# Performance work log

Hardware: AMD Instinct MI355X
Metric: run time of the kernel (lower is better)

The kernel has to match this reference:

```python
import jax, jax.numpy as jnp
import numpy as np

B, C, H, W = 8, 512, 96, 96
C8 = C // 8


def conv1x1(x, w, b):
    # x: (B,Cin,H,W), w: (Cout,Cin), b: (Cout,)
    return jnp.einsum('bchw,oc->bohw', x, w) + b[None, :, None, None]


def setup_inputs() -> dict:
    key = jax.random.key(0)
    ks = jax.random.split(key, 12)
    s = 0.05
    return {
        'x_exmplar': jax.random.normal(ks[0], (B, C, H, W), jnp.float32),
        'x_query': jax.random.normal(ks[1], (B, C, H, W), jnp.float32),
        'Wq': jax.random.normal(ks[2], (C8, C), jnp.float32) * s,
        'bq': jax.random.normal(ks[3], (C8,), jnp.float32) * s,
        'Wk': jax.random.normal(ks[4], (C8, C), jnp.float32) * s,
        'bk': jax.random.normal(ks[5], (C8,), jnp.float32) * s,
        'Wv': jax.random.normal(ks[6], (C, C), jnp.float32) * s,
        'bv': jax.random.normal(ks[7], (C,), jnp.float32) * s,
        'Wqv': jax.random.normal(ks[8], (C, C), jnp.float32) * s,
        'bqv': jax.random.normal(ks[9], (C,), jnp.float32) * s,
        'gamma1': jax.random.normal(ks[10], (1,), jnp.float32) * 0.5,
        'gamma2': jax.random.normal(ks[11], (1,), jnp.float32) * 0.5,
    }


def reference(x_exmplar, x_query, Wq, bq, Wk, bk, Wv, bv, Wqv, bqv, gamma1, gamma2):
    Bq, Cq, Hh, Ww = x_query.shape
    q = conv1x1(x_query, Wq, bq)        # (B,C8,H,W)
    k = conv1x1(x_exmplar, Wk, bk)      # (B,C8,H,W)
    v = conv1x1(x_exmplar, Wv, bv)      # (B,C,H,W)
    qv = conv1x1(x_query, Wqv, bqv)     # (B,C,H,W)

    # Criss-cross energies. energy_H masks the self position (INF diag).
    eH = jnp.einsum('bchw,bcjw->bhwj', q, k)            # (B,H,W,H)
    eye = jnp.eye(Hh, dtype=bool)                        # (H,H)
    eH = jnp.where(eye[:, None, :], -jnp.inf, eH)        # mask h==j
    eW = jnp.einsum('bchw,bchj->bhwj', q, k)             # (B,H,W,W)

    att = jax.nn.softmax(jnp.concatenate([eH, eW], axis=3), axis=3)
    att_H, att_W = att[..., :Hh], att[..., Hh:]          # (B,H,W,H),(B,H,W,W)

    out_H = jnp.einsum('bcjw,bhwj->bchw', v, att_H)
    out_W = jnp.einsum('bchj,bhwj->bchw', v, att_W)
    qout_H = jnp.einsum('bcjw,bhwj->bchw', qv, att_H)
    qout_W = jnp.einsum('bchj,bhwj->bchw', qv, att_W)

    # Diagonal (LR/RL) terms. Note: torch.diagonal of the transposed map equals
    # the diagonal itself, so energy_RL == energy_LR (faithful to original).
    qd = jnp.diagonal(q, axis1=2, axis2=3)               # (B,C8,D)
    kd = jnp.diagonal(k, axis1=2, axis2=3)
    vd = jnp.diagonal(v, axis1=2, axis2=3)               # (B,C,D)
    qvd = jnp.diagonal(qv, axis1=2, axis2=3)
    e_LR = jnp.einsum('bci,bcj->bij', kd, qd)            # (B,D,D)

    # softmax over a size-1 trailing axis (as in the original): yields ones,
    # broadcast-added over the width dim.
    out_LR = jax.nn.softmax(jnp.einsum('bcd,bdj->bcj', vd, e_LR)[..., None], axis=3)
    out_RL = jax.nn.softmax(jnp.einsum('bcd,bdj->bcj', vd, e_LR)[..., None], axis=3)
    qout_LR = jax.nn.softmax(jnp.einsum('bcd,bdj->bcj', qvd, e_LR)[..., None], axis=3)
    qout_RL = jax.nn.softmax(jnp.einsum('bcd,bdj->bcj', qvd, e_LR)[..., None], axis=3)

    examplar_att = out_H + out_W + out_LR + out_RL       # (B,C,H,W) via broadcast
    query_att = qout_H + qout_W + qout_LR + qout_RL
    return (gamma1 * examplar_att + x_exmplar, gamma2 * query_att + x_query)
```

## Files before the change

kernel.cpp:

```cpp
#include <hip/hip_runtime.h>
#include <math.h>

#define C_   512
#define C8_  64
#define HH   96
#define WW   96
#define PP   9216
#define CP   4718592
#define C8P  589824
#define ATTN 1769472

typedef __attribute__((ext_vector_type(4))) float f32x4;
typedef __attribute__((ext_vector_type(8))) __bf16 bf16x8;
typedef __attribute__((ext_vector_type(8))) unsigned short ushort8;
typedef __attribute__((ext_vector_type(4))) unsigned short ushort4v;
typedef __attribute__((ext_vector_type(2))) unsigned short ushort2v;
typedef __attribute__((ext_vector_type(2))) float float2v;

__device__ __forceinline__ float bf2f(unsigned short u) {
    union { unsigned u; float f; } x; x.u = ((unsigned)u) << 16; return x.f;
}
__device__ __forceinline__ unsigned short f2bf(float f) {
    union { float f; unsigned u; } x; x.f = f;
    unsigned r = x.u + 0x7fffu + ((x.u >> 16) & 1u);
    return (unsigned short)(r >> 16);
}
__device__ __forceinline__ void gload16(const void* g, void* l) {
    __builtin_amdgcn_global_load_lds(
        (const __attribute__((address_space(1))) unsigned int*)g,
        (__attribute__((address_space(3))) unsigned int*)l, 16, 0, 0);
}

__global__ __launch_bounds__(256) void cast_w(
    const float* __restrict__ Wv, const float* __restrict__ Wqv,
    const float* __restrict__ Wq, const float* __restrict__ Wk,
    unsigned short* __restrict__ oV, unsigned short* __restrict__ oQV,
    unsigned short* __restrict__ oQ, unsigned short* __restrict__ oK)
{
    int y = blockIdx.y;
    int n = (y < 2) ? 262144 : 32768;
    const float* s = (y == 0) ? Wv : (y == 1) ? Wqv : (y == 2) ? Wq : Wk;
    unsigned short* d = (y == 0) ? oV : (y == 1) ? oQV : (y == 2) ? oQ : oK;
    int i = (blockIdx.x * 256 + threadIdx.x) * 4;
    if (i < n) {
        float4 v = *(const float4*)(s + i);
        ushort4v o = { f2bf(v.x), f2bf(v.y), f2bf(v.z), f2bf(v.w) };
        *(ushort4v*)(d + i) = o;
    }
}

__global__ __launch_bounds__(256) void cast_transpose_cp(
    const float* __restrict__ xq, const float* __restrict__ xe,
    unsigned short* __restrict__ xTq, unsigned short* __restrict__ xTe)
{
    int zz = blockIdx.z;
    int which = zz & 1;
    size_t b = zz >> 1;
    const float* xb = (which ? xe : xq) + b * (size_t)CP;
    unsigned short* xTb = (which ? xTe : xTq) + b * (size_t)CP;
    int p0 = blockIdx.x * 64, c0 = blockIdx.y * 64;

    __shared__ unsigned short T[64][65];
    int t = threadIdx.x;
    int pp = t & 31, cg = t >> 5;
#pragma unroll
    for (int i = 0; i < 8; ++i) {
        int c = cg + 8 * i;
        float2v v = *(const float2v*)(xb + (size_t)(c0 + c) * PP + p0 + pp * 2);
        T[c][pp * 2] = f2bf(v.x);
        T[c][pp * 2 + 1] = f2bf(v.y);
    }
    __syncthreads();
    int cp = t & 31;
#pragma unroll
    for (int i = 0; i < 8; ++i) {
        int e = t + 256 * i;
        int p = e >> 5;
        ushort2v o = { T[cp * 2][p], T[cp * 2 + 1][p] };
        *(ushort2v*)(xTb + (size_t)(p0 + p) * C_ + c0 + cp * 2) = o;
    }
}

__global__ __launch_bounds__(256) void gemm_qk(
    const unsigned short* __restrict__ Wqb, const unsigned short* __restrict__ Wkb,
    const unsigned short* __restrict__ xTq, const unsigned short* __restrict__ xTe,
    const float* __restrict__ bq, const float* __restrict__ bk,
    unsigned short* __restrict__ qout, unsigned short* __restrict__ kout)
{
    int sel = blockIdx.y;
    const unsigned short* A = sel ? Wkb : Wqb;
    const float* bias = sel ? bk : bq;
    int p0 = blockIdx.x * 128;
    size_t b = blockIdx.z;
    const unsigned short* Bb = (sel ? xTe : xTq) + b * (size_t)CP;
    unsigned short* outb = (sel ? kout : qout) + b * (size_t)C8P;

    __shared__ __align__(16) unsigned short Asm[2][64 * 32];
    __shared__ __align__(16) unsigned short Bsm[2][128 * 32];

    int tid = threadIdx.x;
    int lane = tid & 63, wid = tid >> 6;
    int wr = wid >> 1, wc = wid & 1;
    int l15 = lane & 15, l4 = lane >> 4;
    f32x4 acc[2][4] = {};

#define QK_STAGE(KT, BUF)                                                              \
    {                                                                                  \
        int k0s = (KT) * 32;                                                           \
        int c = tid;                                                                   \
        gload16(A + (size_t)(c >> 2) * 512 + k0s + (c & 3) * 8, Asm[BUF] + c * 8);     \
        gload16(Bb + (size_t)(p0 + (c >> 2)) * 512 + k0s + (c & 3) * 8, Bsm[BUF] + c * 8); \
        int cb = tid + 256;                                                            \
        gload16(Bb + (size_t)(p0 + (cb >> 2)) * 512 + k0s + (cb & 3) * 8, Bsm[BUF] + cb * 8); \
    }

    QK_STAGE(0, 0);
    QK_STAGE(1, 1);

#pragma unroll
    for (int k = 0; k < 16; ++k) {
        int cur = k & 1;
        if (k < 15) asm volatile("s_waitcnt vmcnt(3)" ::: "memory");
        else        asm volatile("s_waitcnt vmcnt(0)" ::: "memory");
        __builtin_amdgcn_s_barrier();
        bf16x8 af[2], bfr[4];
#pragma unroll
        for (int m = 0; m < 2; ++m)
            af[m] = *(const bf16x8*)&Asm[cur][(wr * 32 + m * 16 + l15) * 32 + l4 * 8];
#pragma unroll
        for (int n = 0; n < 4; ++n)
            bfr[n] = *(const bf16x8*)&Bsm[cur][(wc * 64 + n * 16 + l15) * 32 + l4 * 8];
#pragma unroll
        for (int m = 0; m < 2; ++m)
#pragma unroll
            for (int n = 0; n < 4; ++n)
                acc[m][n] = __builtin_amdgcn_mfma_f32_16x16x32_bf16(af[m], bfr[n], acc[m][n], 0, 0, 0);
        asm volatile("" ::: "memory");
        __builtin_amdgcn_s_barrier();
        if (k < 14) QK_STAGE(k + 2, cur);
    }
#undef QK_STAGE

#pragma unroll
    for (int m = 0; m < 2; ++m)
#pragma unroll
        for (int n = 0; n < 4; ++n) {
            int pcol = p0 + wc * 64 + n * 16 + l15;
#pragma unroll
            for (int r = 0; r < 4; ++r) {
                int orow = wr * 32 + m * 16 + l4 * 4 + r;
                outb[(size_t)orow * PP + pcol] = f2bf(acc[m][n][r] + bias[orow]);
            }
        }
}

__global__ __launch_bounds__(256) void thw_b(
    const unsigned short* __restrict__ in, unsigned short* __restrict__ out)
{
    size_t m = blockIdx.x;
    const unsigned short* im = in + m * (size_t)PP;
    unsigned short* om = out + m * (size_t)PP;
    __shared__ unsigned short T[96][97];
    int t = threadIdx.x;
#pragma unroll
    for (int i = 0; i < 18; ++i) {
        int v = t + 256 * i;
        int r = v / 48, pp = v - r * 48;
        ushort2v u = *(const ushort2v*)(im + r * 96 + pp * 2);
        T[r][pp * 2] = u.x;
        T[r][pp * 2 + 1] = u.y;
    }
    __syncthreads();
#pragma unroll
    for (int i = 0; i < 18; ++i) {
        int v = t + 256 * i;
        int w = v / 48, hh = v - w * 48;
        ushort2v o = { T[hh * 2][w], T[hh * 2 + 1][w] };
        *(ushort2v*)(om + w * 96 + hh * 2) = o;
    }
}

__global__ __launch_bounds__(256) void scores_kernel(
    const unsigned short* __restrict__ qT, const unsigned short* __restrict__ kT,
    const unsigned short* __restrict__ q, const unsigned short* __restrict__ k,
    unsigned short* __restrict__ attb, float* __restrict__ rsum0, float* __restrict__ rsum1)
{
    int s = blockIdx.x;
    int ori = blockIdx.y;
    size_t b = blockIdx.z;
    const unsigned short* qs = (ori ? q : qT) + b * (size_t)C8P;
    const unsigned short* ks = (ori ? k : kT) + b * (size_t)C8P;
    unsigned short* ab = attb + b * (size_t)ATTN;
    float* rs = (ori ? rsum1 : rsum0) + b * (size_t)PP;

    __shared__ float Qs[64][97];
    __shared__ float Ks[64][97];
    int t = threadIdx.x;
    for (int v = t; v < 64 * 12; v += 256) {
        int c = v / 12, gg = v - c * 12;
        size_t gi = (size_t)c * PP + (size_t)s * 96 + gg * 8;
        ushort8 uq = *(const ushort8*)(qs + gi);
        ushort8 uk = *(const ushort8*)(ks + gi);
#pragma unroll
        for (int kk = 0; kk < 8; ++kk) {
            Qs[c][gg * 8 + kk] = bf2f(uq[kk]);
            Ks[c][gg * 8 + kk] = bf2f(uk[kk]);
        }
    }
    __syncthreads();
    int tx = t & 15, ty = t >> 4;
    float acc[6][6] = {};
    for (int c = 0; c < 64; ++c) {
        float qf[6], kf[6];
#pragma unroll
        for (int i = 0; i < 6; ++i) { qf[i] = Qs[c][ty + 16 * i]; kf[i] = Ks[c][tx + 16 * i]; }
#pragma unroll
        for (int i = 0; i < 6; ++i)
#pragma unroll
            for (int j = 0; j < 6; ++j) acc[i][j] = fmaf(qf[i], kf[j], acc[i][j]);
    }
#pragma unroll
    for (int i = 0; i < 6; ++i) {
        int m = ty + 16 * i;
        size_t row = ori ? ((size_t)s * 96 + m) : ((size_t)m * 96 + s);
        unsigned short* rowp = ab + row * 192 + (ori ? 96 : 0);
        float part = 0.0f;
#pragma unroll
        for (int j = 0; j < 6; ++j) {
            int jj = tx + 16 * j;
            float e = (!ori && jj == m) ? 0.0f : __expf(acc[i][j] - 20.0f);
            part += e;
            rowp[jj] = f2bf(e);
        }
#pragma unroll
        for (int off = 1; off < 16; off <<= 1) part += __shfl_xor(part, off);
        if (tx == 0) rs[row] = part;
    }
}

template<int ORI>
__global__ __launch_bounds__(512) void apply_mfma(
    const unsigned short* __restrict__ xT_e, const unsigned short* __restrict__ xT_q,
    unsigned short* __restrict__ yT_e, unsigned short* __restrict__ yT_q,
    const unsigned short* __restrict__ attb,
    const float* __restrict__ rsum0, const float* __restrict__ rsum1)
{
    int s = blockIdx.x;
    int path = blockIdx.y >> 1, ct = blockIdx.y & 1;
    int c0 = ct * 256;
    size_t b = blockIdx.z;
    const unsigned short* X = (path ? xT_q : xT_e) + b * (size_t)CP;
    unsigned short* Y = (path ? yT_q : yT_e) + b * (size_t)CP;
    const unsigned short* ab = attb + b * (size_t)ATTN;
    const float* r0 = rsum0 + b * (size_t)PP;
    const float* r1 = rsum1 + b * (size_t)PP;

    __shared__ __align__(16) unsigned short Att[96][104];
    __shared__ __align__(16) unsigned short Xs[256][104];

    int tid = threadIdx.x;
    for (int v = tid; v < 96 * 12; v += 512) {
        int r = v / 12, gg = v - r * 12;
        size_t base = ORI ? ((size_t)(s * 96 + r) * 192 + 96) : ((size_t)(r * 96 + s) * 192);
        *(ushort8*)&Att[r][gg * 8] = *(const ushort8*)(ab + base + gg * 8);
    }
    for (int v = tid; v < 96 * 32; v += 512) {
        int j = v >> 5, cc = v & 31;
        size_t pj = ORI ? ((size_t)s * 96 + j) : ((size_t)j * 96 + s);
        ushort8 u = *(const ushort8*)(X + pj * C_ + c0 + cc * 8);
        int js = j ^ ((cc & 3) << 3);
#pragma unroll
        for (int e = 0; e < 8; ++e) Xs[cc * 8 + e][js] = u[e];
    }
    __syncthreads();

    int lane = tid & 63, wid = tid >> 6;
    int wm = wid >> 2, wn = wid & 3;
    int l15 = lane & 15, l4 = lane >> 4;
    f32x4 acc[3][4] = {};
#pragma unroll
    for (int k = 0; k < 3; ++k) {
        bf16x8 a[3], xx[4];
#pragma unroll
        for (int mi = 0; mi < 3; ++mi)
            a[mi] = *(const bf16x8*)&Att[wm * 48 + mi * 16 + l15][k * 32 + l4 * 8];
#pragma unroll
        for (int ni = 0; ni < 4; ++ni) {
            int row = wn * 64 + ni * 16 + l15;
            int gsw = (k * 4 + l4) ^ ((row >> 3) & 3);
            xx[ni] = *(const bf16x8*)&Xs[row][gsw * 8];
        }
#pragma unroll
        for (int mi = 0; mi < 3; ++mi)
#pragma unroll
            for (int ni = 0; ni < 4; ++ni)
                acc[mi][ni] = __builtin_amdgcn_mfma_f32_16x16x32_bf16(a[mi], xx[ni], acc[mi][ni], 0, 0, 0);
    }

#pragma unroll
    for (int mi = 0; mi < 3; ++mi) {
#pragma unroll
        for (int r = 0; r < 4; ++r) {
            int mrow = wm * 48 + mi * 16 + l4 * 4 + r;
            size_t p = ORI ? ((size_t)s * 96 + mrow) : ((size_t)mrow * 96 + s);
            float rinv = 0.0f;
            if (ORI) rinv = 1.0f / (r0[p] + r1[p]);
            size_t base = p * C_ + c0;
#pragma unroll
            for (int ni = 0; ni < 4; ++ni) {
                size_t idx = base + wn * 64 + ni * 16 + l15;
                if (ORI == 0) {
                    Y[idx] = f2bf(acc[mi][ni][r]);
                } else {
                    float tot = bf2f(Y[idx]) + acc[mi][ni][r];
                    Y[idx] = f2bf(tot * rinv);
                }
            }
        }
    }
}

__global__ __launch_bounds__(512) void gemm_out(
    const unsigned short* __restrict__ Wvb, const unsigned short* __restrict__ Wqvb,
    const unsigned short* __restrict__ yT_e, const unsigned short* __restrict__ yT_q,
    const float* __restrict__ bv, const float* __restrict__ bqv,
    const float* __restrict__ xe, const float* __restrict__ xq,
    const float* __restrict__ g1, const float* __restrict__ g2,
    float* __restrict__ o0, float* __restrict__ o1)
{
    int yy = blockIdx.y;
    int path = yy >> 2, ot = yy & 3;
    const unsigned short* A = path ? Wqvb : Wvb;
    const float* bias = path ? bqv : bv;
    int p0 = blockIdx.x * 128;
    int o0r = ot * 128;
    size_t b = blockIdx.z;
    const unsigned short* Bb = (path ? yT_q : yT_e) + b * (size_t)CP;
    const float* xb = (path ? xq : xe) + b * (size_t)CP;
    float* ob = (path ? o1 : o0) + b * (size_t)CP;
    float gam = (path ? g2 : g1)[0];

    __shared__ __align__(16) unsigned short Asm[2][128 * 64];
    __shared__ __align__(16) unsigned short Bsm[2][128 * 64];

    int tid = threadIdx.x;
    int lane = tid & 63, wid = tid >> 6;
    int wr = wid >> 2, wc = wid & 3;
    int l15 = lane & 15, l4 = lane >> 4;
    f32x4 acc[4][2] = {};
    float xv[4][2][4];

#define GO_STAGE(KT, BUF)                                                                  \
    {                                                                                      \
        int k0s = (KT) * 64;                                                               \
        _Pragma("unroll")                                                                  \
        for (int i = 0; i < 2; ++i) {                                                      \
            int ch = tid + i * 512;                                                        \
            int row = ch >> 3, slot = ch & 7;                                              \
            int gs = slot ^ (row & 7);                                                     \
            gload16(A + (size_t)(o0r + row) * 512 + k0s + gs * 8, Asm[BUF] + ch * 8);      \
            gload16(Bb + (size_t)(p0 + row) * 512 + k0s + gs * 8, Bsm[BUF] + ch * 8);      \
        }                                                                                  \
    }

    GO_STAGE(0, 0);
    GO_STAGE(1, 1);

#pragma unroll
    for (int k = 0; k < 8; ++k) {
        int cur = k & 1;
        if (k == 0)      asm volatile("s_waitcnt vmcnt(4)" ::: "memory");
        else if (k < 7)  asm volatile("s_waitcnt vmcnt(8)" ::: "memory");
        else             asm volatile("s_waitcnt vmcnt(4)" ::: "memory");
        __builtin_amdgcn_s_barrier();
#pragma unroll
        for (int ks = 0; ks < 2; ++ks) {
            bf16x8 af[4], bfr[2];
#pragma unroll
            for (int m = 0; m < 4; ++m) {
                int row = wr * 64 + m * 16 + l15;
                int sl = (ks * 4 + l4) ^ (row & 7);
                af[m] = *(const bf16x8*)&Asm[cur][row * 64 + sl * 8];
            }
#pragma unroll
            for (int n = 0; n < 2; ++n) {
                int row = wc * 32 + n * 16 + l15;
                int sl = (ks * 4 + l4) ^ (row & 7);
                bfr[n] = *(const bf16x8*)&Bsm[cur][row * 64 + sl * 8];
            }
#pragma unroll
            for (int m = 0; m < 4; ++m)
#pragma unroll
                for (int n = 0; n < 2; ++n)
                    acc[m][n] = __builtin_amdgcn_mfma_f32_16x16x32_bf16(af[m], bfr[n], acc[m][n], 0, 0, 0);
        }
        asm volatile("" ::: "memory");
        __builtin_amdgcn_s_barrier();
        {
            int xm = k >> 1, xn = k & 1;
            int pcol = p0 + wc * 32 + xn * 16 + l15;
#pragma unroll
            for (int r = 0; r < 4; ++r) {
                int orow = o0r + wr * 64 + xm * 16 + l4 * 4 + r;
                xv[xm][xn][r] = xb[(size_t)orow * PP + pcol];
            }
        }
        if (k < 6) GO_STAGE(k + 2, cur);
    }
#undef GO_STAGE
    asm volatile("s_waitcnt vmcnt(0)" ::: "memory");

#pragma unroll
    for (int m = 0; m < 4; ++m)
#pragma unroll
        for (int n = 0; n < 2; ++n) {
            int pcol = p0 + wc * 32 + n * 16 + l15;
#pragma unroll
            for (int r = 0; r < 4; ++r) {
                int orow = o0r + wr * 64 + m * 16 + l4 * 4 + r;
                size_t idx = (size_t)orow * PP + pcol;
                float val = acc[m][n][r] + bias[orow];
                ob[idx] = gam * (val + 2.0f) + xv[m][n][r];
            }
        }
}

extern "C" void kernel_launch(void* const* d_in, const int* in_sizes, int n_in,
                              void* d_out, int out_size, void* d_ws, size_t ws_size,
                              hipStream_t stream)
{
    const float* x_ex = (const float*)d_in[0];
    const float* x_q  = (const float*)d_in[1];
    const float* Wq   = (const float*)d_in[2];
    const float* bq   = (const float*)d_in[3];
    const float* Wk   = (const float*)d_in[4];
    const float* bk   = (const float*)d_in[5];
    const float* Wv   = (const float*)d_in[6];
    const float* bv   = (const float*)d_in[7];
    const float* Wqv  = (const float*)d_in[8];
    const float* bqv  = (const float*)d_in[9];
    const float* g1   = (const float*)d_in[10];
    const float* g2   = (const float*)d_in[11];
    float* out0 = (float*)d_out;
    float* out1 = out0 + (size_t)8 * CP;

    unsigned short* hp = (unsigned short*)d_ws;
    unsigned short* Wvb  = hp; hp += 262144;
    unsigned short* Wqvb = hp; hp += 262144;
    unsigned short* Wqb  = hp; hp += 32768;
    unsigned short* Wkb  = hp; hp += 32768;
    size_t head = (size_t)(hp - (unsigned short*)d_ws) * 2;

    size_t perB = 4ull * CP + (size_t)ATTN + 4ull * C8P + 4ull * PP;
    int g = 8;
    while (g > 1 && head + (size_t)g * perB * 2 > ws_size) g >>= 1;

    unsigned short* p = hp;
    unsigned short* xT_e = p; p += (size_t)g * CP;
    unsigned short* xT_q = p; p += (size_t)g * CP;
    unsigned short* yT_e = p; p += (size_t)g * CP;
    unsigned short* yT_q = p; p += (size_t)g * CP;
    unsigned short* attb = p; p += (size_t)g * ATTN;
    unsigned short* qb   = p; p += (size_t)g * C8P;
    unsigned short* kb   = p; p += (size_t)g * C8P;
    unsigned short* qTb  = p; p += (size_t)g * C8P;
    unsigned short* kTb  = p; p += (size_t)g * C8P;
    float* rsum0 = (float*)p; p += (size_t)g * PP * 2;
    float* rsum1 = (float*)p; p += (size_t)g * PP * 2;

    cast_w<<<dim3(256, 4), 256, 0, stream>>>(Wv, Wqv, Wq, Wk, Wvb, Wqvb, Wqb, Wkb);

    for (int b0 = 0; b0 < 8; b0 += g) {
        const float* xe = x_ex + (size_t)b0 * CP;
        const float* xq = x_q  + (size_t)b0 * CP;
        float* o0 = out0 + (size_t)b0 * CP;
        float* o1 = out1 + (size_t)b0 * CP;

        cast_transpose_cp<<<dim3(144, 8, 2 * g), 256, 0, stream>>>(xq, xe, xT_q, xT_e);
        gemm_qk<<<dim3(72, 2, g), 256, 0, stream>>>(Wqb, Wkb, xT_q, xT_e, bq, bk, qb, kb);
        thw_b<<<dim3(2 * g * 64), 256, 0, stream>>>(qb, qTb);
        scores_kernel<<<dim3(96, 2, g), 256, 0, stream>>>(qTb, kTb, qb, kb, attb, rsum0, rsum1);
        apply_mfma<0><<<dim3(96, 4, g), 512, 0, stream>>>(xT_e, xT_q, yT_e, yT_q, attb, rsum0, rsum1);
        apply_mfma<1><<<dim3(96, 4, g), 512, 0, stream>>>(xT_e, xT_q, yT_e, yT_q, attb, rsum0, rsum1);
        gemm_out<<<dim3(72, 8, g), 512, 0, stream>>>(Wvb, Wqvb, yT_e, yT_q, bv, bqv,
                                                     xe, xq, g1, g2, o0, o1);
    }
}
```

Baseline: 561.4 us.

## Stage apply_mfma epilogue through LDS for vectorized stores; remap gemm_out block order

The apply_mfma epilogue now writes the MFMA accumulators as bf16 into shared memory, reusing the Xs buffer, and then writes whole 16-byte rows to global memory. The read-modify-write path reads whole rows and uses per-row reciprocal sums precomputed in LDS. Before, each lane did scattered 2-byte stores and loads and recomputed the reciprocal per element. Separately, gemm_out remaps its linear block index so that the 8 blocks sharing a linear residue are grouped. The aim is better L2 locality or spread across XCDs, at the cost of two extra barriers and an LDS round trip.

```diff
diff --git a/kernel.cpp b/kernel.cpp
--- a/kernel.cpp
+++ b/kernel.cpp
@@ -257,6 +257,7 @@
 
     __shared__ __align__(16) unsigned short Att[96][104];
     __shared__ __align__(16) unsigned short Xs[256][104];
+    __shared__ float rs_[96];
 
     int tid = threadIdx.x;
     for (int v = tid; v < 96 * 12; v += 512) {
@@ -272,6 +273,10 @@
 #pragma unroll
         for (int e = 0; e < 8; ++e) Xs[cc * 8 + e][js] = u[e];
     }
+    if (ORI && tid < 96) {
+        size_t p = (size_t)s * 96 + tid;
+        rs_[tid] = 1.0f / (r0[p] + r1[p]);
+    }
     __syncthreads();
 
     int lane = tid & 63, wid = tid >> 6;
@@ -297,25 +302,38 @@
                 acc[mi][ni] = __builtin_amdgcn_mfma_f32_16x16x32_bf16(a[mi], xx[ni], acc[mi][ni], 0, 0, 0);
     }
 
-#pragma unroll
-    for (int mi = 0; mi < 3; ++mi) {
+    unsigned short* Wf = &Xs[0][0];
+    __syncthreads();
+#pragma unroll
+    for (int mi = 0; mi < 3; ++mi)
 #pragma unroll
         for (int r = 0; r < 4; ++r) {
             int mrow = wm * 48 + mi * 16 + l4 * 4 + r;
-            size_t p = ORI ? ((size_t)s * 96 + mrow) : ((size_t)mrow * 96 + s);
-            float rinv = 0.0f;
-            if (ORI) rinv = 1.0f / (r0[p] + r1[p]);
-            size_t base = p * C_ + c0;
-#pragma unroll
-            for (int ni = 0; ni < 4; ++ni) {
-                size_t idx = base + wn * 64 + ni * 16 + l15;
-                if (ORI == 0) {
-                    Y[idx] = f2bf(acc[mi][ni][r]);
-                } else {
-                    float tot = bf2f(Y[idx]) + acc[mi][ni][r];
-                    Y[idx] = f2bf(tot * rinv);
-                }
-            }
+#pragma unroll
+            for (int ni = 0; ni < 4; ++ni)
+                Wf[mrow * 268 + wn * 64 + ni * 16 + l15] = f2bf(acc[mi][ni][r]);
+        }
+    __syncthreads();
+#pragma unroll
+    for (int i = 0; i < 6; ++i) {
+        int id = tid + 512 * i;
+        int row = id >> 5, cg = id & 31;
+        ushort4v w0 = *(const ushort4v*)&Wf[row * 268 + cg * 8];
+        ushort4v w1 = *(const ushort4v*)&Wf[row * 268 + cg * 8 + 4];
+        size_t p = ORI ? ((size_t)s * 96 + row) : ((size_t)row * 96 + s);
+        unsigned short* yp = Y + p * C_ + c0 + cg * 8;
+        if (ORI == 0) {
+            ushort8 o = { w0[0], w0[1], w0[2], w0[3], w1[0], w1[1], w1[2], w1[3] };
+            *(ushort8*)yp = o;
+        } else {
+            ushort8 yo = *(const ushort8*)yp;
+            float rinv = rs_[row];
+            ushort8 o;
+#pragma unroll
+            for (int e = 0; e < 4; ++e) o[e] = f2bf((bf2f(yo[e]) + bf2f(w0[e])) * rinv);
+#pragma unroll
+            for (int e = 0; e < 4; ++e) o[e + 4] = f2bf((bf2f(yo[e + 4]) + bf2f(w1[e])) * rinv);
+            *(ushort8*)yp = o;
         }
     }
 }
@@ -328,11 +346,15 @@
     const float* __restrict__ g1, const float* __restrict__ g2,
     float* __restrict__ o0, float* __restrict__ o1)
 {
-    int yy = blockIdx.y;
-    int path = yy >> 2, ot = yy & 3;
+    int lin = blockIdx.x + 72 * blockIdx.y;
+    int nid = (lin & 7) * 72 + (lin >> 3);
+    int path = nid / 288;
+    int rem = nid - path * 288;
+    int ptile = rem >> 2, ot = rem & 3;
+
     const unsigned short* A = path ? Wqvb : Wvb;
     const float* bias = path ? bqv : bv;
-    int p0 = blockIdx.x * 128;
+    int p0 = ptile * 128;
     int o0r = ot * 128;
     size_t b = blockIdx.z;
     const unsigned short* Bb = (path ? yT_q : yT_e) + b * (size_t)CP;
```

Result: faster. 545.6 us (-2.8%).
